# Kernel optimization log

Hardware: AMD Instinct MI355X
Metric: run time of the kernel (lower is better)

Reference implementation:

```python
import jax, jax.numpy as jnp
import numpy as np

B, T, L, H = 512, 512, 64, 512  # batch, time_steps, sequence_len, hidden_dim


def gru_cell(x, h, W_ih, W_hh, b_ih, b_hh):
    # PyTorch GRUCell math. W_ih: [3H, in], W_hh: [3H, H]; gate order (r, z, n).
    gi = x @ W_ih.T + b_ih
    gh = h @ W_hh.T + b_hh
    i_r, i_z, i_n = jnp.split(gi, 3, axis=-1)
    h_r, h_z, h_n = jnp.split(gh, 3, axis=-1)
    r = jax.nn.sigmoid(i_r + h_r)
    z = jax.nn.sigmoid(i_z + h_z)
    n = jnp.tanh(i_n + r * h_n)
    return (1.0 - z) * n + z * h


def setup_inputs() -> dict:
    key = jax.random.key(0)
    ks = jax.random.split(key, 12)
    s = 1.0 / np.sqrt(H)  # PyTorch GRUCell/Linear init scale
    u = lambda k, shape: jax.random.uniform(k, shape, jnp.float32, -s, s)
    return {
        "x": jax.random.normal(ks[0], (B, T + L - 1), jnp.float32),
        "h_1": jnp.zeros((B, H), jnp.float32),
        "h_2": jnp.zeros((B, H), jnp.float32),
        "W_ih1": u(ks[1], (3 * H, T)),
        "W_hh1": u(ks[2], (3 * H, H)),
        "b_ih1": u(ks[3], (3 * H,)),
        "b_hh1": u(ks[4], (3 * H,)),
        "W_ih2": u(ks[5], (3 * H, H)),
        "W_hh2": u(ks[6], (3 * H, H)),
        "b_ih2": u(ks[7], (3 * H,)),
        "b_hh2": u(ks[8], (3 * H,)),
        "W_fc": u(ks[9], (1, H)),
        "b_fc": u(ks[10], (1,)),
    }


def reference(x, h_1, h_2, W_ih1, W_hh1, b_ih1, b_hh1,
              W_ih2, W_hh2, b_ih2, b_hh2, W_fc, b_fc):
    # Sliding windows x[:, t:t+T] for t in [0, L): gather once, scan over steps.
    idx = jnp.arange(L)[:, None] + jnp.arange(T)[None, :]  # [L, T]
    xs = jnp.transpose(x[:, idx], (1, 0, 2))  # [L, B, T]

    def step(carry, x_t):
        h1, h2 = carry
        h1 = gru_cell(x_t, h1, W_ih1, W_hh1, b_ih1, b_hh1)
        h2 = gru_cell(h1, h2, W_ih2, W_hh2, b_ih2, b_hh2)
        y = (h2 @ W_fc.T + b_fc)[:, 0]  # [B]
        return (h1, h2), y

    (h1, h2), ys = jax.lax.scan(step, (h_1, h_2), xs)
    return ys.T, h1, h2  # output_seq [B, L], final hidden states
```

## Files before the change

kernel.cpp:

```cpp
#include <hip/hip_runtime.h>
#include <hip/hip_bf16.h>
#include <math.h>

typedef __attribute__((ext_vector_type(8))) short short8;
typedef __attribute__((ext_vector_type(4))) float f32x4;
typedef __attribute__((ext_vector_type(4))) int i32x4;
typedef unsigned short u16;
typedef unsigned int u32;
typedef unsigned long long u64;

__device__ __forceinline__ u16 f2bf(float f) {
  union { float f; u32 u; } x; x.f = f;
  return (u16)((x.u + 0x7fffu + ((x.u >> 16) & 1u)) >> 16);
}
__device__ __forceinline__ float bf2f(u32 bits) {
  union { u32 u; float f; } x; x.u = bits; return x.f;
}
__device__ __forceinline__ float sigm(float v) { return 1.0f / (1.0f + __expf(-v)); }

#define MFMA __builtin_amdgcn_mfma_f32_16x16x32_bf16
#define HS 262144

#define LDG16_BODY(FL)                                        \
    "global_load_dwordx4 %0, %16, off " FL "\n\t"             \
    "global_load_dwordx4 %1, %16, off offset:64 " FL "\n\t"   \
    "global_load_dwordx4 %2, %16, off offset:128 " FL "\n\t"  \
    "global_load_dwordx4 %3, %16, off offset:192 " FL "\n\t"  \
    "global_load_dwordx4 %4, %16, off offset:256 " FL "\n\t"  \
    "global_load_dwordx4 %5, %16, off offset:320 " FL "\n\t"  \
    "global_load_dwordx4 %6, %16, off offset:384 " FL "\n\t"  \
    "global_load_dwordx4 %7, %16, off offset:448 " FL "\n\t"  \
    "global_load_dwordx4 %8, %16, off offset:512 " FL "\n\t"  \
    "global_load_dwordx4 %9, %16, off offset:576 " FL "\n\t"  \
    "global_load_dwordx4 %10, %16, off offset:640 " FL "\n\t" \
    "global_load_dwordx4 %11, %16, off offset:704 " FL "\n\t" \
    "global_load_dwordx4 %12, %16, off offset:768 " FL "\n\t" \
    "global_load_dwordx4 %13, %16, off offset:832 " FL "\n\t" \
    "global_load_dwordx4 %14, %16, off offset:896 " FL "\n\t" \
    "global_load_dwordx4 %15, %16, off offset:960 " FL "\n\t" \
    "s_waitcnt vmcnt(0)"
#define LDG16_OPS(a, base)                                                     \
    : "=&v"(a[0]), "=&v"(a[1]), "=&v"(a[2]), "=&v"(a[3]), "=&v"(a[4]),         \
      "=&v"(a[5]), "=&v"(a[6]), "=&v"(a[7]), "=&v"(a[8]), "=&v"(a[9]),         \
      "=&v"(a[10]), "=&v"(a[11]), "=&v"(a[12]), "=&v"(a[13]), "=&v"(a[14]),    \
      "=&v"(a[15])                                                             \
    : "v"(base) : "memory"

__device__ __forceinline__ void ldg16_sc0(short8 a[16], const u16* base) {
  asm volatile(LDG16_BODY("sc0") LDG16_OPS(a, base));
}
__device__ __forceinline__ void ldg16_sc01(short8 a[16], const u16* base) {
  asm volatile(LDG16_BODY("sc0 sc1") LDG16_OPS(a, base));
}
__device__ __forceinline__ void stg4_sc01(void* p, i32x4 v) {
  asm volatile("global_store_dwordx4 %0, %1, off sc0 sc1" :: "v"(p), "v"(v) : "memory");
}
__device__ __forceinline__ void stg1_sc01(void* p, u32 v) {
  asm volatile("global_store_dword %0, %1, off sc0 sc1" :: "v"(p), "v"(v) : "memory");
}

__device__ __forceinline__ void waitpair(const u64* p, u32 tlo, u32 thi) {
  while (true) {
    u64 v = __hip_atomic_load(p, __ATOMIC_RELAXED, __HIP_MEMORY_SCOPE_AGENT);
    if ((u32)v >= tlo && (u32)(v >> 32) >= thi) return;
    __builtin_amdgcn_s_sleep(1);
  }
}

__global__ __launch_bounds__(256, 1) void gru_fused(
    const float* __restrict__ xin, const float* __restrict__ h1in, const float* __restrict__ h2in,
    const float* __restrict__ Wih1, const float* __restrict__ Whh1,
    const float* __restrict__ bih1, const float* __restrict__ bhh1,
    const float* __restrict__ Wih2, const float* __restrict__ Whh2,
    const float* __restrict__ bih2, const float* __restrict__ bhh2,
    const float* __restrict__ Wfc, const float* __restrict__ bfc,
    float* __restrict__ out, u16* __restrict__ wsb, unsigned* __restrict__ barc)
{
  const int bid   = blockIdx.x;
  const int rb    = bid & 3;
  const int layer = (bid >> 2) & 1;
  const int cbl   = bid >> 3;
  const int n0    = cbl * 16;
  const int wid   = bid >> 2;
  const int tid   = threadIdx.x;
  const int w     = tid >> 6;
  const int lane  = tid & 63;
  const int quad  = lane >> 4;
  const int m16   = lane & 15;

  u16* x0  = wsb;
  u16* x1  = x0 + 512 * 576;
  u16* h1r = x1 + 512 * 576;
  u16* h2r = h1r + 4 * HS;
  u16* h1m = h2r + 4 * HS;
  u32* ysl = (u32*)(h1m + 4 * HS);

  __shared__ short8 wlds[96 * 64];
  __shared__ u32 stage[4 * 288];

  u64* pair = (u64*)(barc + rb * 16);
  u32* c0   = (u32*)pair;
  u32* c1   = c0 + 1;
  u32* cinit = barc + 128;
  u32* cfin  = barc + 132;

  const float* Wih = layer ? Wih2 : Wih1;
  const float* Whh = layer ? Whh2 : Whh1;
  const float* bih = layer ? bih2 : bih1;
  const float* bhh = layer ? bhh2 : bhh1;

  for (int i = wid * 256 + tid; i < 128 * 575; i += 64 * 256) {
    int r = i / 575, c = i - r * 575;
    int row = rb * 128 + r;
    u16 bv = f2bf(xin[row * 575 + c]);
    x0[row * 576 + c] = bv;
    if (c >= 1) x1[row * 576 + (c - 1)] = bv;
  }
  for (int i = wid * 256 + tid; i < 128 * 512; i += 64 * 256) {
    int r = i >> 9, c = i & 511;
    int row = rb * 128 + r;
    h1r[3 * HS + row * 512 + c] = f2bf(h1in[row * 512 + c]);
    h2r[3 * HS + row * 512 + c] = f2bf(h2in[row * 512 + c]);
  }
  for (int i = tid; i < 96 * 64; i += 256) {
    int blk = i >> 6, l = i & 63;
    int s, gr;
    if (blk < 64) { s = blk & 31; gr = (blk >> 5) * 512; }
    else          { s = blk - 64; gr = 1024; }
    int n  = n0 + (l & 15);
    int k0 = s * 32 + (l >> 4) * 8;
    short8 pk;
    #pragma unroll
    for (int j = 0; j < 8; ++j) {
      int k = k0 + j;
      float v = (k < 512) ? Wih[(gr + n) * 512 + k] : Whh[(gr + n) * 512 + (k - 512)];
      pk[j] = (short)f2bf(v);
    }
    wlds[blk * 64 + l] = pk;
  }

  float hreg[2][4];
  const float* hin = layer ? h2in : h1in;
  #pragma unroll
  for (int rf = 0; rf < 2; ++rf)
    #pragma unroll
    for (int q = 0; q < 4; ++q)
      hreg[rf][q] = hin[(rb * 128 + (2 * w + rf) * 16 + quad * 4 + q) * 512 + n0 + m16];

  const int nn = n0 + m16;
  const float bias_r  = bih[nn] + bhh[nn];
  const float bias_z  = bih[512 + nn] + bhh[512 + nn];
  const float bias_in = bih[1024 + nn];
  const float bias_hn = bhh[1024 + nn];
  const float bfcv = bfc[0];
  float wfc8[8];
  #pragma unroll
  for (int k = 0; k < 8; ++k) wfc8[k] = Wfc[n0 + (lane & 1) * 8 + k];

  __syncthreads();
  if (tid == 0) {
    __builtin_amdgcn_fence(__ATOMIC_RELEASE, "agent");
    __hip_atomic_fetch_add(cinit, 1u, __ATOMIC_RELAXED, __HIP_MEMORY_SCOPE_AGENT);
    while (__hip_atomic_load(cinit, __ATOMIC_RELAXED, __HIP_MEMORY_SCOPE_AGENT) < 256u)
      __builtin_amdgcn_s_sleep(1);
    __builtin_amdgcn_fence(__ATOMIC_ACQUIRE, "agent");
  }
  __syncthreads();

  const int arow0 = rb * 128 + (2 * w) * 16 + m16;
  const int arow1 = arow0 + 16;
  const int rl    = lane >> 1;
  const int hl    = lane & 1;
  const int growt = rb * 128 + w * 32 + rl;

  if (layer == 0) {
    for (int u = 0; u < 64; ++u) {
      f32x4 acc[2][4] = {};
      {
        const int c = u & 1;
        const u16* xc = c ? x1 : x0;
        const u32* pa0 = (const u32*)(xc + (size_t)arow0 * 576 + (u - c) + quad * 8);
        const u32* pa1 = (const u32*)(xc + (size_t)arow1 * 576 + (u - c) + quad * 8);
        #pragma unroll
        for (int s = 0; s < 16; ++s) {
          union { short8 v; u32 u4[4]; } a0, a1;
          #pragma unroll
          for (int j = 0; j < 4; ++j) { a0.u4[j] = pa0[s * 16 + j]; a1.u4[j] = pa1[s * 16 + j]; }
          short8 br = wlds[(s)      * 64 + lane];
          short8 bz = wlds[(32 + s) * 64 + lane];
          short8 bi = wlds[(64 + s) * 64 + lane];
          acc[0][0] = MFMA(a0.v, br, acc[0][0], 0, 0, 0);
          acc[1][0] = MFMA(a1.v, br, acc[1][0], 0, 0, 0);
          acc[0][1] = MFMA(a0.v, bz, acc[0][1], 0, 0, 0);
          acc[1][1] = MFMA(a1.v, bz, acc[1][1], 0, 0, 0);
          acc[0][2] = MFMA(a0.v, bi, acc[0][2], 0, 0, 0);
          acc[1][2] = MFMA(a1.v, bi, acc[1][2], 0, 0, 0);
        }
      }
      waitpair(pair, 32u * (unsigned)u, u >= 4 ? 32u * (unsigned)(u - 3) : 0u);
      #pragma unroll
      for (int rf = 0; rf < 2; ++rf) {
        short8 a[16];
        const u16* base = h1r + (size_t)((u + 3) & 3) * HS +
                          (size_t)(rf ? arow1 : arow0) * 512 + quad * 8;
        ldg16_sc0(a, base);
        #pragma unroll
        for (int s = 0; s < 16; ++s) {
          short8 br = wlds[(16 + s) * 64 + lane];
          short8 bz = wlds[(48 + s) * 64 + lane];
          short8 bh = wlds[(80 + s) * 64 + lane];
          acc[rf][0] = MFMA(a[s], br, acc[rf][0], 0, 0, 0);
          acc[rf][1] = MFMA(a[s], bz, acc[rf][1], 0, 0, 0);
          acc[rf][3] = MFMA(a[s], bh, acc[rf][3], 0, 0, 0);
        }
      }
      #pragma unroll
      for (int rf = 0; rf < 2; ++rf)
        #pragma unroll
        for (int q = 0; q < 4; ++q) {
          float rg = sigm(acc[rf][0][q] + bias_r);
          float zg = sigm(acc[rf][1][q] + bias_z);
          float ng = tanhf(acc[rf][2][q] + bias_in + rg * (acc[rf][3][q] + bias_hn));
          float hv = (1.0f - zg) * ng + zg * hreg[rf][q];
          hreg[rf][q] = hv;
          u16 b = f2bf(hv);
          u32 pv = (u32)b | ((u32)(u16)__shfl_xor((int)b, 1) << 16);
          if (!(m16 & 1))
            stage[w * 288 + (rf * 16 + quad * 4 + q) * 9 + (m16 >> 1)] = pv;
        }
      {
        i32x4 dv;
        dv.x = (int)stage[w * 288 + rl * 9 + hl * 4 + 0];
        dv.y = (int)stage[w * 288 + rl * 9 + hl * 4 + 1];
        dv.z = (int)stage[w * 288 + rl * 9 + hl * 4 + 2];
        dv.w = (int)stage[w * 288 + rl * 9 + hl * 4 + 3];
        size_t off = (size_t)(u & 3) * HS + (size_t)growt * 512 + n0 + hl * 8;
        *(i32x4*)(h1r + off) = dv;
        stg4_sc01(h1m + off, dv);
      }
      asm volatile("s_waitcnt vmcnt(0)" ::: "memory");
      __syncthreads();
      if (tid == 0)
        __hip_atomic_fetch_add(c0, 1u, __ATOMIC_RELAXED, __HIP_MEMORY_SCOPE_AGENT);
    }
  } else {
    for (int v = 0; v < 64; ++v) {
      f32x4 acc[2][4] = {};
      waitpair(pair, 32u * (unsigned)(v + 1), 32u * (unsigned)v);
      #pragma unroll
      for (int rf = 0; rf < 2; ++rf) {
        short8 a[16];
        const u16* base = h2r + (size_t)((v + 3) & 3) * HS +
                          (size_t)(rf ? arow1 : arow0) * 512 + quad * 8;
        ldg16_sc0(a, base);
        #pragma unroll
        for (int s = 0; s < 16; ++s) {
          short8 br = wlds[(16 + s) * 64 + lane];
          short8 bz = wlds[(48 + s) * 64 + lane];
          short8 bh = wlds[(80 + s) * 64 + lane];
          acc[rf][0] = MFMA(a[s], br, acc[rf][0], 0, 0, 0);
          acc[rf][1] = MFMA(a[s], bz, acc[rf][1], 0, 0, 0);
          acc[rf][3] = MFMA(a[s], bh, acc[rf][3], 0, 0, 0);
        }
      }
      #pragma unroll
      for (int rf = 0; rf < 2; ++rf) {
        short8 a[16];
        const u16* base = h1m + (size_t)(v & 3) * HS +
                          (size_t)(rf ? arow1 : arow0) * 512 + quad * 8;
        ldg16_sc01(a, base);
        #pragma unroll
        for (int s = 0; s < 16; ++s) {
          short8 br = wlds[(s)      * 64 + lane];
          short8 bz = wlds[(32 + s) * 64 + lane];
          short8 bi = wlds[(64 + s) * 64 + lane];
          acc[rf][0] = MFMA(a[s], br, acc[rf][0], 0, 0, 0);
          acc[rf][1] = MFMA(a[s], bz, acc[rf][1], 0, 0, 0);
          acc[rf][2] = MFMA(a[s], bi, acc[rf][2], 0, 0, 0);
        }
      }
      #pragma unroll
      for (int rf = 0; rf < 2; ++rf)
        #pragma unroll
        for (int q = 0; q < 4; ++q) {
          float rg = sigm(acc[rf][0][q] + bias_r);
          float zg = sigm(acc[rf][1][q] + bias_z);
          float ng = tanhf(acc[rf][2][q] + bias_in + rg * (acc[rf][3][q] + bias_hn));
          float hv = (1.0f - zg) * ng + zg * hreg[rf][q];
          hreg[rf][q] = hv;
          u16 b = f2bf(hv);
          u32 pv = (u32)b | ((u32)(u16)__shfl_xor((int)b, 1) << 16);
          if (!(m16 & 1))
            stage[w * 288 + (rf * 16 + quad * 4 + q) * 9 + (m16 >> 1)] = pv;
        }
      {
        i32x4 dv;
        dv.x = (int)stage[w * 288 + rl * 9 + hl * 4 + 0];
        dv.y = (int)stage[w * 288 + rl * 9 + hl * 4 + 1];
        dv.z = (int)stage[w * 288 + rl * 9 + hl * 4 + 2];
        dv.w = (int)stage[w * 288 + rl * 9 + hl * 4 + 3];
        size_t off = (size_t)(v & 3) * HS + (size_t)growt * 512 + n0 + hl * 8;
        *(i32x4*)(h2r + off) = dv;
        float yl = 0.0f;
        u32 dd[4] = {(u32)dv.x, (u32)dv.y, (u32)dv.z, (u32)dv.w};
        #pragma unroll
        for (int j = 0; j < 4; ++j) {
          yl += bf2f(dd[j] << 16) * wfc8[2 * j];
          yl += bf2f(dd[j] & 0xffff0000u) * wfc8[2 * j + 1];
        }
        yl += __shfl_xor(yl, 1);
        if (!hl) {
          union { float f; u32 u; } yu; yu.f = yl;
          stg1_sc01(ysl + ((size_t)(cbl * 512 + growt) * 64 + v), yu.u);
        }
      }
      asm volatile("s_waitcnt vmcnt(0)" ::: "memory");
      __syncthreads();
      if (tid == 0)
        __hip_atomic_fetch_add(c1, 1u, __ATOMIC_RELAXED, __HIP_MEMORY_SCOPE_AGENT);
    }
  }

  float* hout = out + 32768 + layer * (512 * 512);
  #pragma unroll
  for (int rf = 0; rf < 2; ++rf)
    #pragma unroll
    for (int q = 0; q < 4; ++q) {
      int row = rb * 128 + (2 * w + rf) * 16 + quad * 4 + q;
      hout[row * 512 + nn] = hreg[rf][q];
    }

  asm volatile("s_waitcnt vmcnt(0)" ::: "memory");
  __syncthreads();
  if (tid == 0)
    __hip_atomic_fetch_add(cfin, 1u, __ATOMIC_RELAXED, __HIP_MEMORY_SCOPE_AGENT);
  while (__hip_atomic_load(cfin, __ATOMIC_RELAXED, __HIP_MEMORY_SCOPE_AGENT) < 256u)
    __builtin_amdgcn_s_sleep(1);

  if (tid < 128) {
    int row = 2 * bid + (tid >> 6);
    int t   = tid & 63;
    float acc = bfcv;
    #pragma unroll
    for (int cb = 0; cb < 32; ++cb) {
      u32 bits = __hip_atomic_load(ysl + ((size_t)(cb * 512 + row) * 64 + t),
                                   __ATOMIC_RELAXED, __HIP_MEMORY_SCOPE_AGENT);
      union { u32 u; float f; } cv; cv.u = bits;
      acc += cv.f;
    }
    out[row * 64 + t] = acc;
  }
}

extern "C" void kernel_launch(void* const* d_in, const int* in_sizes, int n_in,
                              void* d_out, int out_size, void* d_ws, size_t ws_size,
                              hipStream_t stream) {
  (void)in_sizes; (void)n_in; (void)out_size; (void)ws_size;
  (void)hipMemsetAsync(d_ws, 0, 4096, stream);
  unsigned* bar = (unsigned*)d_ws;
  u16* wsb = (u16*)((char*)d_ws + 4096);
  gru_fused<<<256, 256, 0, stream>>>(
      (const float*)d_in[0], (const float*)d_in[1], (const float*)d_in[2],
      (const float*)d_in[3], (const float*)d_in[4], (const float*)d_in[5], (const float*)d_in[6],
      (const float*)d_in[7], (const float*)d_in[8], (const float*)d_in[9], (const float*)d_in[10],
      (const float*)d_in[11], (const float*)d_in[12],
      (float*)d_out, wsb, bar);
}
```

Before: 930.9 us.

## Replace atomic counter barrier with per-block flags and batch h loads

Replaces the shared atomic-add counters per row-block with per-block flag words that each block writes with a plain coherent store. Waiters poll all 64 flags at once, one lane per flag, and proceed when all are satisfied. This is meant to remove contention on the atomic counters. Separately, the two 16-load batches of hidden-state rows are merged into one 32-load batch with a single wait, so more loads are in flight and the MFMAs of the two row fragments interleave. The cost is higher register pressure and more polling traffic.

```diff
diff --git a/kernel.cpp b/kernel.cpp
--- a/kernel.cpp
+++ b/kernel.cpp
@@ -21,36 +21,55 @@
 #define MFMA __builtin_amdgcn_mfma_f32_16x16x32_bf16
 #define HS 262144
 
-#define LDG16_BODY(FL)                                        \
-    "global_load_dwordx4 %0, %16, off " FL "\n\t"             \
-    "global_load_dwordx4 %1, %16, off offset:64 " FL "\n\t"   \
-    "global_load_dwordx4 %2, %16, off offset:128 " FL "\n\t"  \
-    "global_load_dwordx4 %3, %16, off offset:192 " FL "\n\t"  \
-    "global_load_dwordx4 %4, %16, off offset:256 " FL "\n\t"  \
-    "global_load_dwordx4 %5, %16, off offset:320 " FL "\n\t"  \
-    "global_load_dwordx4 %6, %16, off offset:384 " FL "\n\t"  \
-    "global_load_dwordx4 %7, %16, off offset:448 " FL "\n\t"  \
-    "global_load_dwordx4 %8, %16, off offset:512 " FL "\n\t"  \
-    "global_load_dwordx4 %9, %16, off offset:576 " FL "\n\t"  \
-    "global_load_dwordx4 %10, %16, off offset:640 " FL "\n\t" \
-    "global_load_dwordx4 %11, %16, off offset:704 " FL "\n\t" \
-    "global_load_dwordx4 %12, %16, off offset:768 " FL "\n\t" \
-    "global_load_dwordx4 %13, %16, off offset:832 " FL "\n\t" \
-    "global_load_dwordx4 %14, %16, off offset:896 " FL "\n\t" \
-    "global_load_dwordx4 %15, %16, off offset:960 " FL "\n\t" \
+#define LDG32_BODY(FL)                                         \
+    "global_load_dwordx4 %0, %32, off " FL "\n\t"              \
+    "global_load_dwordx4 %1, %32, off offset:64 " FL "\n\t"    \
+    "global_load_dwordx4 %2, %32, off offset:128 " FL "\n\t"   \
+    "global_load_dwordx4 %3, %32, off offset:192 " FL "\n\t"   \
+    "global_load_dwordx4 %4, %32, off offset:256 " FL "\n\t"   \
+    "global_load_dwordx4 %5, %32, off offset:320 " FL "\n\t"   \
+    "global_load_dwordx4 %6, %32, off offset:384 " FL "\n\t"   \
+    "global_load_dwordx4 %7, %32, off offset:448 " FL "\n\t"   \
+    "global_load_dwordx4 %8, %32, off offset:512 " FL "\n\t"   \
+    "global_load_dwordx4 %9, %32, off offset:576 " FL "\n\t"   \
+    "global_load_dwordx4 %10, %32, off offset:640 " FL "\n\t"  \
+    "global_load_dwordx4 %11, %32, off offset:704 " FL "\n\t"  \
+    "global_load_dwordx4 %12, %32, off offset:768 " FL "\n\t"  \
+    "global_load_dwordx4 %13, %32, off offset:832 " FL "\n\t"  \
+    "global_load_dwordx4 %14, %32, off offset:896 " FL "\n\t"  \
+    "global_load_dwordx4 %15, %32, off offset:960 " FL "\n\t"  \
+    "global_load_dwordx4 %16, %33, off " FL "\n\t"             \
+    "global_load_dwordx4 %17, %33, off offset:64 " FL "\n\t"   \
+    "global_load_dwordx4 %18, %33, off offset:128 " FL "\n\t"  \
+    "global_load_dwordx4 %19, %33, off offset:192 " FL "\n\t"  \
+    "global_load_dwordx4 %20, %33, off offset:256 " FL "\n\t"  \
+    "global_load_dwordx4 %21, %33, off offset:320 " FL "\n\t"  \
+    "global_load_dwordx4 %22, %33, off offset:384 " FL "\n\t"  \
+    "global_load_dwordx4 %23, %33, off offset:448 " FL "\n\t"  \
+    "global_load_dwordx4 %24, %33, off offset:512 " FL "\n\t"  \
+    "global_load_dwordx4 %25, %33, off offset:576 " FL "\n\t"  \
+    "global_load_dwordx4 %26, %33, off offset:640 " FL "\n\t"  \
+    "global_load_dwordx4 %27, %33, off offset:704 " FL "\n\t"  \
+    "global_load_dwordx4 %28, %33, off offset:768 " FL "\n\t"  \
+    "global_load_dwordx4 %29, %33, off offset:832 " FL "\n\t"  \
+    "global_load_dwordx4 %30, %33, off offset:896 " FL "\n\t"  \
+    "global_load_dwordx4 %31, %33, off offset:960 " FL "\n\t"  \
     "s_waitcnt vmcnt(0)"
-#define LDG16_OPS(a, base)                                                     \
+#define LDG32_OPS(a, b0, b1)                                                   \
     : "=&v"(a[0]), "=&v"(a[1]), "=&v"(a[2]), "=&v"(a[3]), "=&v"(a[4]),         \
       "=&v"(a[5]), "=&v"(a[6]), "=&v"(a[7]), "=&v"(a[8]), "=&v"(a[9]),         \
       "=&v"(a[10]), "=&v"(a[11]), "=&v"(a[12]), "=&v"(a[13]), "=&v"(a[14]),    \
-      "=&v"(a[15])                                                             \
-    : "v"(base) : "memory"
-
-__device__ __forceinline__ void ldg16_sc0(short8 a[16], const u16* base) {
-  asm volatile(LDG16_BODY("sc0") LDG16_OPS(a, base));
-}
-__device__ __forceinline__ void ldg16_sc01(short8 a[16], const u16* base) {
-  asm volatile(LDG16_BODY("sc0 sc1") LDG16_OPS(a, base));
+      "=&v"(a[15]), "=&v"(a[16]), "=&v"(a[17]), "=&v"(a[18]), "=&v"(a[19]),    \
+      "=&v"(a[20]), "=&v"(a[21]), "=&v"(a[22]), "=&v"(a[23]), "=&v"(a[24]),    \
+      "=&v"(a[25]), "=&v"(a[26]), "=&v"(a[27]), "=&v"(a[28]), "=&v"(a[29]),    \
+      "=&v"(a[30]), "=&v"(a[31])                                               \
+    : "v"(b0), "v"(b1) : "memory"
+
+__device__ __forceinline__ void ldg32_sc0(short8 a[32], const u16* b0, const u16* b1) {
+  asm volatile(LDG32_BODY("sc0") LDG32_OPS(a, b0, b1));
+}
+__device__ __forceinline__ void ldg32_sc01(short8 a[32], const u16* b0, const u16* b1) {
+  asm volatile(LDG32_BODY("sc0 sc1") LDG32_OPS(a, b0, b1));
 }
 __device__ __forceinline__ void stg4_sc01(void* p, i32x4 v) {
   asm volatile("global_store_dwordx4 %0, %1, off sc0 sc1" :: "v"(p), "v"(v) : "memory");
@@ -58,13 +77,22 @@
 __device__ __forceinline__ void stg1_sc01(void* p, u32 v) {
   asm volatile("global_store_dword %0, %1, off sc0 sc1" :: "v"(p), "v"(v) : "memory");
 }
-
-__device__ __forceinline__ void waitpair(const u64* p, u32 tlo, u32 thi) {
-  while (true) {
-    u64 v = __hip_atomic_load(p, __ATOMIC_RELAXED, __HIP_MEMORY_SCOPE_AGENT);
-    if ((u32)v >= tlo && (u32)(v >> 32) >= thi) return;
-    __builtin_amdgcn_s_sleep(1);
-  }
+__device__ __forceinline__ void stflag(u32* p, u32 v) {
+  asm volatile("global_store_dword %0, %1, off sc0 sc1\n\ts_waitcnt vmcnt(0)"
+               :: "v"(p), "v"(v) : "memory");
+}
+__device__ __forceinline__ u32 ldflag(const u32* p) {
+  u32 v;
+  asm volatile("global_load_dword %0, %1, off sc0 sc1\n\ts_waitcnt vmcnt(0)"
+               : "=v"(v) : "v"(p) : "memory");
+  return v;
+}
+
+__device__ __forceinline__ void waitflags(const u32* f, int lane, u32 t0, u32 t1) {
+  const u32* p = f + lane;
+  const u32 tgt = (lane < 32) ? t0 : t1;
+  while (!__all((int)(ldflag(p) >= tgt)))
+    __builtin_amdgcn_s_sleep(2);
 }
 
 __global__ __launch_bounds__(256, 1) void gru_fused(
@@ -98,11 +126,10 @@
   __shared__ short8 wlds[96 * 64];
   __shared__ u32 stage[4 * 288];
 
-  u64* pair = (u64*)(barc + rb * 16);
-  u32* c0   = (u32*)pair;
-  u32* c1   = c0 + 1;
-  u32* cinit = barc + 128;
-  u32* cfin  = barc + 132;
+  u32* flags  = barc + rb * 64;
+  u32* myflag = flags + (layer ? 32 : 0) + cbl;
+  u32* cinit  = barc + 320;
+  u32* cfin   = barc + 324;
 
   const float* Wih = layer ? Wih2 : Wih1;
   const float* Whh = layer ? Whh2 : Whh1;
@@ -197,21 +224,23 @@
           acc[1][2] = MFMA(a1.v, bi, acc[1][2], 0, 0, 0);
         }
       }
-      waitpair(pair, 32u * (unsigned)u, u >= 4 ? 32u * (unsigned)(u - 3) : 0u);
-      #pragma unroll
-      for (int rf = 0; rf < 2; ++rf) {
-        short8 a[16];
-        const u16* base = h1r + (size_t)((u + 3) & 3) * HS +
-                          (size_t)(rf ? arow1 : arow0) * 512 + quad * 8;
-        ldg16_sc0(a, base);
+      waitflags(flags, lane, (u32)u, u >= 4 ? (u32)(u - 3) : 0u);
+      {
+        short8 a[32];
+        const u16* slab = h1r + (size_t)((u + 3) & 3) * HS;
+        ldg32_sc0(a, slab + (size_t)arow0 * 512 + quad * 8,
+                     slab + (size_t)arow1 * 512 + quad * 8);
         #pragma unroll
         for (int s = 0; s < 16; ++s) {
           short8 br = wlds[(16 + s) * 64 + lane];
           short8 bz = wlds[(48 + s) * 64 + lane];
           short8 bh = wlds[(80 + s) * 64 + lane];
-          acc[rf][0] = MFMA(a[s], br, acc[rf][0], 0, 0, 0);
-          acc[rf][1] = MFMA(a[s], bz, acc[rf][1], 0, 0, 0);
-          acc[rf][3] = MFMA(a[s], bh, acc[rf][3], 0, 0, 0);
+          acc[0][0] = MFMA(a[s], br, acc[0][0], 0, 0, 0);
+          acc[1][0] = MFMA(a[16 + s], br, acc[1][0], 0, 0, 0);
+          acc[0][1] = MFMA(a[s], bz, acc[0][1], 0, 0, 0);
+          acc[1][1] = MFMA(a[16 + s], bz, acc[1][1], 0, 0, 0);
+          acc[0][3] = MFMA(a[s], bh, acc[0][3], 0, 0, 0);
+          acc[1][3] = MFMA(a[16 + s], bh, acc[1][3], 0, 0, 0);
         }
       }
       #pragma unroll
@@ -240,43 +269,46 @@
       }
       asm volatile("s_waitcnt vmcnt(0)" ::: "memory");
       __syncthreads();
-      if (tid == 0)
-        __hip_atomic_fetch_add(c0, 1u, __ATOMIC_RELAXED, __HIP_MEMORY_SCOPE_AGENT);
+      if (tid == 0) stflag(myflag, (u32)(u + 1));
     }
   } else {
     for (int v = 0; v < 64; ++v) {
       f32x4 acc[2][4] = {};
-      waitpair(pair, 32u * (unsigned)(v + 1), 32u * (unsigned)v);
-      #pragma unroll
-      for (int rf = 0; rf < 2; ++rf) {
-        short8 a[16];
-        const u16* base = h2r + (size_t)((v + 3) & 3) * HS +
-                          (size_t)(rf ? arow1 : arow0) * 512 + quad * 8;
-        ldg16_sc0(a, base);
+      waitflags(flags, lane, (u32)(v + 1), (u32)v);
+      {
+        short8 a[32];
+        const u16* slab = h2r + (size_t)((v + 3) & 3) * HS;
+        ldg32_sc0(a, slab + (size_t)arow0 * 512 + quad * 8,
+                     slab + (size_t)arow1 * 512 + quad * 8);
         #pragma unroll
         for (int s = 0; s < 16; ++s) {
           short8 br = wlds[(16 + s) * 64 + lane];
           short8 bz = wlds[(48 + s) * 64 + lane];
           short8 bh = wlds[(80 + s) * 64 + lane];
-          acc[rf][0] = MFMA(a[s], br, acc[rf][0], 0, 0, 0);
-          acc[rf][1] = MFMA(a[s], bz, acc[rf][1], 0, 0, 0);
-          acc[rf][3] = MFMA(a[s], bh, acc[rf][3], 0, 0, 0);
-        }
-      }
-      #pragma unroll
-      for (int rf = 0; rf < 2; ++rf) {
-        short8 a[16];
-        const u16* base = h1m + (size_t)(v & 3) * HS +
-                          (size_t)(rf ? arow1 : arow0) * 512 + quad * 8;
-        ldg16_sc01(a, base);
+          acc[0][0] = MFMA(a[s], br, acc[0][0], 0, 0, 0);
+          acc[1][0] = MFMA(a[16 + s], br, acc[1][0], 0, 0, 0);
+          acc[0][1] = MFMA(a[s], bz, acc[0][1], 0, 0, 0);
+          acc[1][1] = MFMA(a[16 + s], bz, acc[1][1], 0, 0, 0);
+          acc[0][3] = MFMA(a[s], bh, acc[0][3], 0, 0, 0);
+          acc[1][3] = MFMA(a[16 + s], bh, acc[1][3], 0, 0, 0);
+        }
+      }
+      {
+        short8 a[32];
+        const u16* slab = h1m + (size_t)(v & 3) * HS;
+        ldg32_sc01(a, slab + (size_t)arow0 * 512 + quad * 8,
+                      slab + (size_t)arow1 * 512 + quad * 8);
         #pragma unroll
         for (int s = 0; s < 16; ++s) {
           short8 br = wlds[(s)      * 64 + lane];
           short8 bz = wlds[(32 + s) * 64 + lane];
           short8 bi = wlds[(64 + s) * 64 + lane];
-          acc[rf][0] = MFMA(a[s], br, acc[rf][0], 0, 0, 0);
-          acc[rf][1] = MFMA(a[s], bz, acc[rf][1], 0, 0, 0);
-          acc[rf][2] = MFMA(a[s], bi, acc[rf][2], 0, 0, 0);
+          acc[0][0] = MFMA(a[s], br, acc[0][0], 0, 0, 0);
+          acc[1][0] = MFMA(a[16 + s], br, acc[1][0], 0, 0, 0);
+          acc[0][1] = MFMA(a[s], bz, acc[0][1], 0, 0, 0);
+          acc[1][1] = MFMA(a[16 + s], bz, acc[1][1], 0, 0, 0);
+          acc[0][2] = MFMA(a[s], bi, acc[0][2], 0, 0, 0);
+          acc[1][2] = MFMA(a[16 + s], bi, acc[1][2], 0, 0, 0);
         }
       }
       #pragma unroll
@@ -316,8 +348,7 @@
       }
       asm volatile("s_waitcnt vmcnt(0)" ::: "memory");
       __syncthreads();
-      if (tid == 0)
-        __hip_atomic_fetch_add(c1, 1u, __ATOMIC_RELAXED, __HIP_MEMORY_SCOPE_AGENT);
+      if (tid == 0) stflag(myflag, (u32)(v + 1));
     }
   }
 
```

New measurement: 848.1 us. -8.9%, faster.
